# Kernel optimization log

Measured on AMD Instinct MI355X. Metric: run time of the kernel, lower is better.

The kernel has to match this reference:

```python
import jax, jax.numpy as jnp
import numpy as np
from jax import lax


def conv1x1(x, w, b):
    # x [B,Ci,H,W], w [Co,Ci], b [Co]
    return jnp.einsum('oi,bihw->bohw', w, x) + b[None, :, None, None]


def dil_conv_relu(x, w, b):
    # 3x3 conv, dilation 2, padding 2 (make_layers with dilation=True), then ReLU
    y = lax.conv_general_dilated(x, w, (1, 1), [(2, 2), (2, 2)], rhs_dilation=(2, 2),
                                 dimension_numbers=('NCHW', 'OIHW', 'NCHW'))
    return jax.nn.relu(y + b[None, :, None, None])


def conv1d_relu(x, w, b):
    # x [n,c,L], w [o,i,9], padding 4 -> same length; conv + ReLU (nn.Sequential(Conv2d, ReLU))
    y = lax.conv_general_dilated(x, w, (1,), [(4, 4)], dimension_numbers=('NCH', 'OIH', 'NCH'))
    return jax.nn.relu(y + b[None, :, None])


def dulr_pass(slices, w, b):
    # slices [L,n,c,m]; out[0]=slices[0]; out[i]=convrelu(out[i-1]) + slices[i]
    def step(carry, s):
        new = conv1d_relu(carry, w, b) + s
        return new, new
    _, rest = lax.scan(step, slices[0], slices[1:])
    return jnp.concatenate([slices[:1], rest], axis=0)


def conv_du(x, w, b):
    # down pass then up pass over rows (kernel (1,9) -> 1D conv along width)
    rows = jnp.moveaxis(x, 2, 0)            # [h,n,c,w]
    rows = dulr_pass(rows, w, b)
    rows = dulr_pass(rows[::-1], w, b)[::-1]
    return jnp.moveaxis(rows, 0, 2)


def conv_lr(x, w, b):
    # left-right then right-left over columns (kernel (9,1) -> 1D conv along height)
    cols = jnp.moveaxis(x, 3, 0)            # [w,n,c,h]
    cols = dulr_pass(cols, w, b)
    cols = dulr_pass(cols[::-1], w, b)[::-1]
    return jnp.moveaxis(cols, 0, 3)


def setup_inputs() -> dict:
    key = jax.random.key(0)
    ks = jax.random.split(key, 24)
    B, H, W = 4, 64, 64
    std = 0.01
    f32 = jnp.float32
    d = {}
    d['in_data'] = jax.random.normal(ks[0], (B, 1025, H, W), f32)
    d['wA'] = jax.random.normal(ks[1], (128, 1024), f32) * std
    d['bA'] = jax.random.normal(ks[2], (128,), f32) * std
    d['wB'] = jax.random.normal(ks[3], (128, 1024), f32) * std
    d['bB'] = jax.random.normal(ks[4], (128,), f32) * std
    d['wC'] = jax.random.normal(ks[5], (1024, 1024), f32) * std
    d['bC'] = jax.random.normal(ks[6], (1024,), f32) * std
    d['gamma'] = jnp.array(0.1, f32)
    chans = [(512, 1024), (512, 512), (512, 512), (256, 512), (128, 256), (64, 128)]
    for i, (co, ci) in enumerate(chans):
        d[f'bw{i+1}'] = jax.random.normal(ks[7 + 2 * i], (co, ci, 3, 3), f32) * std
        d[f'bb{i+1}'] = jax.random.normal(ks[8 + 2 * i], (co,), f32) * std
    d['du_w'] = jax.random.normal(ks[19], (64, 64, 9), f32) * std
    d['du_b'] = jax.random.normal(ks[20], (64,), f32) * std
    d['lr_w'] = jax.random.normal(ks[21], (64, 64, 9), f32) * std
    d['lr_b'] = jax.random.normal(ks[22], (64,), f32) * std
    d['ow'] = jax.random.normal(ks[23], (1, 64), f32) * std
    d['ob'] = jnp.zeros((1,), f32)
    return d


def reference(in_data, wA, bA, wB, bB, wC, bC, gamma,
              bw1, bb1, bw2, bb2, bw3, bb3, bw4, bb4, bw5, bb5, bw6, bb6,
              du_w, du_b, lr_w, lr_b, ow, ob):
    x = in_data[:, :1024]                   # [B,1024,H,W]
    f = in_data[:, 1024:1025]               # [B,1,H,W]
    B, C, H, W = x.shape
    N = H * W
    # appearance_A(x) -> query [B,128,N]
    q = conv1x1(x, wA, bA).reshape(B, 128, N)
    # f1024 = f broadcast to 1024 channels; flow_B(f1024) (1x1 conv) == f * sum_i wB[:,i] + bB
    k = (f * wB.sum(axis=1)[None, :, None, None] + bB[None, :, None, None]).reshape(B, 128, N)
    energy = jnp.einsum('bcn,bcm->bnm', q, k)           # [B,N,N] = q^T k
    att = jax.nn.softmax(energy, axis=-1)
    v = conv1x1(x, wC, bC).reshape(B, C, N)             # appearance_C
    out = jnp.einsum('bcj,bij->bci', v, att).reshape(B, C, H, W)  # bmm(v, att^T)
    x = gamma * out + x
    for w_, b_ in ((bw1, bb1), (bw2, bb2), (bw3, bb3), (bw4, bb4), (bw5, bb5), (bw6, bb6)):
        x = dil_conv_relu(x, w_, b_)
    x = conv_du(x, du_w, du_b)
    x = conv_lr(x, lr_w, lr_b)
    x = jax.nn.relu(conv1x1(x, ow, ob))                 # o_layer
    # F.upsample(scale_factor=8) default nearest
    x = jnp.repeat(jnp.repeat(x, 8, axis=2), 8, axis=3)
    return x
```

## Files before the change

### kernel.cpp

```cpp
#include <hip/hip_runtime.h>


#define NPIX 4096

typedef _Float16 f16;
typedef _Float16 f16x8 __attribute__((ext_vector_type(8)));
typedef _Float16 f16x4 __attribute__((ext_vector_type(4)));
typedef float f32x4 __attribute__((ext_vector_type(4)));

__device__ inline void async16(const void* g, void* l) {
  __builtin_amdgcn_global_load_lds(
      (const __attribute__((address_space(1))) unsigned int*)g,
      (__attribute__((address_space(3))) unsigned int*)l, 16, 0, 0);
}


__global__ void rf_zero(float* __restrict__ z) { z[threadIdx.x] = 0.f; }

__global__ void rf_s(const float* __restrict__ wB, const float* __restrict__ bA,
                     float* __restrict__ s_out, float* __restrict__ c0_out) {
  int c = threadIdx.x;
  const float* row = wB + (size_t)c * 1024;
  float acc = 0.f;
  for (int i = 0; i < 1024; ++i) acc += row[i];
  s_out[c] = acc;
  __shared__ float sh[128];
  sh[c] = acc * bA[c];
  __syncthreads();
  for (int off = 64; off > 0; off >>= 1) {
    if (c < off) sh[c] += sh[c + off];
    __syncthreads();
  }
  if (c == 0) c0_out[0] = sh[0];
}

__global__ void rf_u(const float* __restrict__ wA, const float* __restrict__ s,
                     float* __restrict__ u) {
  int i = blockIdx.x * 256 + threadIdx.x;
  float acc = 0.f;
  for (int c = 0; c < 128; ++c) acc += s[c] * wA[(size_t)c * 1024 + i];
  u[i] = acc;
}

__global__ void rf_fstat(const float* __restrict__ in, float* __restrict__ fstat) {
  int b = blockIdx.x;
  int t = threadIdx.x;
  const float* f = in + ((size_t)b * 1025 + 1024) * NPIX;
  float mx = -1e30f, mn = 1e30f;
  for (int j = t; j < NPIX; j += 256) {
    float v = f[j];
    mx = fmaxf(mx, v);
    mn = fminf(mn, v);
  }
  __shared__ float smx[256], smn[256];
  smx[t] = mx; smn[t] = mn;
  __syncthreads();
  for (int off = 128; off > 0; off >>= 1) {
    if (t < off) {
      smx[t] = fmaxf(smx[t], smx[t + off]);
      smn[t] = fminf(smn[t], smn[t + off]);
    }
    __syncthreads();
  }
  if (t == 0) { fstat[b] = smx[0]; fstat[4 + b] = smn[0]; }
}

__global__ __launch_bounds__(256) void rf_A(const float* __restrict__ in,
                                            const float* __restrict__ u,
                                            const float* __restrict__ c0p,
                                            const float* __restrict__ fst,
                                            float* __restrict__ A, float* __restrict__ M) {
  __shared__ float ul[1024];
  int b = blockIdx.y;
  int n = blockIdx.x * 256 + threadIdx.x;
  for (int s = threadIdx.x; s < 1024; s += 256) ul[s] = u[s];
  __syncthreads();
  const float* xp = in + (size_t)b * 1025 * NPIX + n;
  float acc = c0p[0];
#pragma unroll 8
  for (int i = 0; i < 1024; ++i) acc = fmaf(ul[i], xp[(size_t)i * NPIX], acc);
  A[b * NPIX + n] = acc;
  M[b * NPIX + n] = fmaxf(acc * fst[b], acc * fst[4 + b]);
}

__global__ void rf_Z(const float* __restrict__ in, const float* __restrict__ A,
                     const float* __restrict__ M, float* __restrict__ iZ) {
  int idx = blockIdx.x * 4 + (threadIdx.x >> 6);
  int lane = threadIdx.x & 63;
  int b = idx >> 12;
  const float* f = in + ((size_t)b * 1025 + 1024) * NPIX;
  float a = A[idx], m = M[idx];
  float acc = 0.f;
#pragma unroll 4
  for (int it = 0; it < 64; ++it) acc += __expf(a * f[lane + it * 64] - m);
  for (int off = 32; off > 0; off >>= 1) acc += __shfl_down(acc, off, 64);
  if (lane == 0) iZ[idx] = 1.0f / acc;
}


__global__ void rf_xsplit(const float* __restrict__ in, f16* __restrict__ xh) {
  __shared__ float tl[64][65];
  int nt = blockIdx.x, ct = blockIdx.y, b = blockIdx.z;
  int n0 = nt * 64, c0 = ct * 64;
  int tid = threadIdx.x;
  for (int s = tid; s < 4096; s += 256) {
    int r = s >> 6, c = s & 63;
    tl[r][c] = in[((size_t)b * 1025 + c0 + r) * NPIX + n0 + c];
  }
  __syncthreads();
  for (int s = tid; s < 512; s += 256) {
    int n = s >> 3, g = s & 7;
    f16x8 hb;
#pragma unroll
    for (int q = 0; q < 8; ++q) hb[q] = (f16)(16.f * tl[g * 8 + q][n]);
    size_t o = ((size_t)b * NPIX + n0 + n) * 1024 + c0 + g * 8;
    *(f16x8*)&xh[o] = hb;
  }
}


__global__ void rf_wC1(const float* __restrict__ wC, f16* __restrict__ wh) {
  int base = (blockIdx.x * 256 + threadIdx.x) * 8;
  f16x8 hb;
#pragma unroll
  for (int q = 0; q < 8; ++q) hb[q] = (f16)(256.f * wC[base + q]);
  *(f16x8*)&wh[base] = hb;
}


__global__ __launch_bounds__(256, 2) void rf_vgemmm(
    const f16* __restrict__ wh, const f16* __restrict__ xh,
    const float* __restrict__ bC, f16* __restrict__ vH) {
  __shared__ f16 sA[2][4096], sB[2][4096];
  const int tid = threadIdx.x;
  const int nb = blockIdx.x * 128, cb = blockIdx.y * 128, b = blockIdx.z;
  const int pA = tid & 127;
  const int wv = tid >> 6, lane = tid & 63;
  const int mrow = lane & 15, quad = lane >> 4;
  const int wm = (wv & 1) * 64, wn = (wv >> 1) * 64;
  const size_t abase = (size_t)(cb + pA) * 1024;
  const size_t bbase = ((size_t)b * NPIX + nb + pA) * 1024;
  f32x4 acc[4][4];
#pragma unroll
  for (int i = 0; i < 4; ++i)
#pragma unroll
    for (int j = 0; j < 4; ++j) acc[i][j] = (f32x4){0.f, 0.f, 0.f, 0.f};

  auto stage = [&](int k0, int pb) {
#pragma unroll
    for (int s = 0; s < 2; ++s) {
      const int cc = ((tid + 256 * s) >> 7) & 3;
      const int lb = ((tid & ~63) + 256 * s) * 8;
      async16(wh + abase + k0 + cc * 8, &sA[pb][lb]);
      async16(xh + bbase + k0 + cc * 8, &sB[pb][lb]);
    }
  };
  stage(0, 0);
  int p = 0;
  for (int k0 = 0; k0 < 1024; k0 += 32) {
    __syncthreads();
    if (k0 + 32 < 1024) stage(k0 + 32, p ^ 1);
    f16x8 fa[4], fb[4];
#pragma unroll
    for (int mi = 0; mi < 4; ++mi)
      fa[mi] = *(const f16x8*)&sA[p][(quad * 128 + wm + mi * 16 + mrow) * 8];
#pragma unroll
    for (int ni = 0; ni < 4; ++ni)
      fb[ni] = *(const f16x8*)&sB[p][(quad * 128 + wn + ni * 16 + mrow) * 8];
#pragma unroll
    for (int mi = 0; mi < 4; ++mi)
#pragma unroll
      for (int ni = 0; ni < 4; ++ni)
        acc[mi][ni] = __builtin_amdgcn_mfma_f32_16x16x32_f16(fa[mi], fb[ni], acc[mi][ni], 0, 0, 0);
    p ^= 1;
  }
  const float inv = 1.0f / 4096.0f;
#pragma unroll
  for (int mi = 0; mi < 4; ++mi) {
#pragma unroll
    for (int rg = 0; rg < 4; ++rg) {
      int c = cb + wm + mi * 16 + quad * 4 + rg;
      float bv = bC[c];
#pragma unroll
      for (int ni = 0; ni < 4; ++ni) {
        int j = nb + wn + ni * 16 + mrow;
        vH[((size_t)b * 1024 + c) * NPIX + j] =
            (f16)(16.f * (acc[mi][ni][rg] * inv + bv));
      }
    }
  }
}


__global__ __launch_bounds__(256, 2) void rf_attm(
    const f16* __restrict__ vH,
    const float* __restrict__ Aarr, const float* __restrict__ Marr,
    const float* __restrict__ iZ, const float* __restrict__ in,
    const float* __restrict__ gptr, f16* __restrict__ yH) {
  __shared__ f16 sAh[4096], sPh[4096];
  const int tid = threadIdx.x;
  const int ib = blockIdx.x * 128, cb = blockIdx.y * 128, b = blockIdx.z;
  const int pA = tid & 127;
  const int wv = tid >> 6, lane = tid & 63;
  const int mrow = lane & 15, quad = lane >> 4;
  const int wm = (wv & 1) * 64, wn = (wv >> 1) * 64;
  const size_t vbase = ((size_t)b * 1024 + cb + pA) * NPIX;
  const int ni_ = tid & 127;
  const int kc0 = tid >> 7;
  const float av = Aarr[b * NPIX + ib + ni_];
  const float mv = Marr[b * NPIX + ib + ni_];
  const float zv = iZ[b * NPIX + ib + ni_] * 16.f;
  const float* f = in + ((size_t)b * 1025 + 1024) * NPIX;
  f32x4 acc[4][4];
#pragma unroll
  for (int i = 0; i < 4; ++i)
#pragma unroll
    for (int j = 0; j < 4; ++j) acc[i][j] = (f32x4){0.f, 0.f, 0.f, 0.f};
  for (int j0 = 0; j0 < NPIX; j0 += 32) {
#pragma unroll
    for (int s = 0; s < 2; ++s) {
      const int cc = ((tid + 256 * s) >> 7) & 3;
      const int lb = ((tid & ~63) + 256 * s) * 8;
      async16(vH + vbase + j0 + cc * 8, &sAh[lb]);
    }
#pragma unroll
    for (int it = 0; it < 2; ++it) {
      const int kc = kc0 + 2 * it;
      const float4 fa = *(const float4*)&f[j0 + kc * 8];
      const float4 fb = *(const float4*)&f[j0 + kc * 8 + 4];
      const float fj[8] = {fa.x, fa.y, fa.z, fa.w, fb.x, fb.y, fb.z, fb.w};
      f16x8 ph;
#pragma unroll
      for (int q = 0; q < 8; ++q)
        ph[q] = (f16)(__expf(fmaf(av, fj[q], -mv)) * zv);
      *(f16x8*)&sPh[(kc * 128 + ni_) * 8] = ph;
    }
    __syncthreads();
    f16x8 fa[4], fb[4];
#pragma unroll
    for (int mi = 0; mi < 4; ++mi)
      fa[mi] = *(const f16x8*)&sAh[(quad * 128 + wm + mi * 16 + mrow) * 8];
#pragma unroll
    for (int ni = 0; ni < 4; ++ni)
      fb[ni] = *(const f16x8*)&sPh[(quad * 128 + wn + ni * 16 + mrow) * 8];
#pragma unroll
    for (int mi = 0; mi < 4; ++mi)
#pragma unroll
      for (int ni = 0; ni < 4; ++ni)
        acc[mi][ni] = __builtin_amdgcn_mfma_f32_16x16x32_f16(fa[mi], fb[ni], acc[mi][ni], 0, 0, 0);
    __syncthreads();
  }
  const float g = gptr[0];
  const float inv = 1.0f / 256.0f;
#pragma unroll
  for (int mi = 0; mi < 4; ++mi) {
    const int cbase = cb + wm + mi * 16 + quad * 4;
#pragma unroll
    for (int ni = 0; ni < 4; ++ni) {
      const int i = ib + wn + ni * 16 + mrow;
      f16x4 hv;
#pragma unroll
      for (int rg = 0; rg < 4; ++rg) {
        float xr = in[((size_t)b * 1025 + cbase + rg) * NPIX + i];
        hv[rg] = (f16)(16.f * (g * (acc[mi][ni][rg] * inv) + xr));
      }
      *(f16x4*)&yH[((size_t)b * NPIX + i) * 1024 + cbase] = hv;
    }
  }
}


__global__ void rf_wfragc(const float* __restrict__ w, f16* __restrict__ F,
                          int CI, int CO) {
  int gid = blockIdx.x * 256 + threadIdx.x;
  const int C16 = CO >> 4, KI = CI >> 5;
  const int total = 9 * KI * C16 * 64;
  if (gid >= total) return;
  int lane = gid & 63;
  int rest = gid >> 6;
  int c16 = rest % C16;
  int rest2 = rest / C16;
  int k = rest2 % KI;
  int t = rest2 / KI;
  int co = c16 * 16 + (lane & 15);
  int ci = k * 32 + (lane >> 4) * 8;
  f16x8 hb;
#pragma unroll
  for (int j = 0; j < 8; ++j)
    hb[j] = (f16)(256.0f * w[((size_t)co * CI + ci + j) * 9 + t]);
  *(f16x8*)&F[(size_t)gid * 8] = hb;
}


template <int BM, int BN, bool F32OUT>
__global__ __launch_bounds__(256, 2) void rf_mconv(
    const f16* __restrict__ xh, const f16* __restrict__ F,
    const float* __restrict__ bias, const float* __restrict__ zp,
    f16* __restrict__ oh, float* __restrict__ of, int CI, int CO) {
  constexpr int ROWS = BM / 64;
  constexpr int TPI = 4096 / BM;
  constexpr int HROWS = ROWS + 4;
  constexpr int COLP = 72;
  constexpr int CHUNKS = HROWS * 4 * COLP;
  constexpr int NSTG = (CHUNKS + 255) / 256;
  __shared__ f16 sA[2][NSTG * 2048];
  const int tid = threadIdx.x;
  const int blkpx = blockIdx.x;
  const int cob = blockIdx.y * BN;
  const int b = blkpx / TPI;
  const int h0 = (blkpx - b * TPI) * ROWS;

  const int wv = tid >> 6, lane = tid & 63;
  const int mrow = lane & 15, quad = lane >> 4;
  const int wm = (BN == 128) ? (wv & 1) * 64 : wv * 64;
  const int wn = (BN == 128) ? (wv >> 1) * 64 : 0;
  const int r_out = wm >> 6;
  const int KI = CI >> 5;
  const int C16 = CO >> 4;
  const int cb16 = (cob + wn) >> 4;

  f32x4 acc[4][4];
#pragma unroll
  for (int i = 0; i < 4; ++i)
#pragma unroll
    for (int j = 0; j < 4; ++j) acc[i][j] = (f32x4){0.f, 0.f, 0.f, 0.f};

  const f16* abase[NSTG];
  unsigned vmask = 0;
#pragma unroll
  for (int s = 0; s < NSTG; ++s) {
    int idx = tid + 256 * s;
    int rowks = idx / COLP;
    int col = idx - rowks * COLP;
    int r = rowks >> 2, ks = rowks & 3;
    int srow = h0 + r - 2, scol = col - 2;
    bool ok = (idx < CHUNKS) && ((unsigned)srow < 64u) && ((unsigned)scol < 64u);
    abase[s] = ok ? xh + (((size_t)b * 64 + srow) * 64 + scol) * CI + ks * 8
                  : (const f16*)zp;
    if (ok) vmask |= (1u << s);
  }
  auto stageA = [&](int k, int pb) {
#pragma unroll
    for (int s = 0; s < NSTG; ++s) {
      const f16* sp = abase[s] + (((vmask >> s) & 1u) ? k * 32 : 0);
      async16(sp, &sA[pb][((tid & ~63) + 256 * s) * 8]);
    }
  };

  const f16* Fb = F + ((size_t)cb16 * 64 + lane) * 8;

  stageA(0, 0);
  int p = 0;
  for (int k = 0; k < KI; ++k) {
    __syncthreads();
    if (k + 1 < KI) stageA(k + 1, p ^ 1);
#pragma unroll
    for (int t = 0; t < 9; ++t) {
      const int dh = (t / 3) * 2 - 2, dw = (t - (t / 3) * 3) * 2 - 2;
      f16x8 fb[4];
#pragma unroll
      for (int ni = 0; ni < 4; ++ni)
        fb[ni] = *(const f16x8*)(Fb + ((size_t)(t * KI + k) * C16 + ni) * 512);
      f16x8 fa[4];
#pragma unroll
      for (int mi = 0; mi < 4; ++mi)
        fa[mi] = *(const f16x8*)&sA[p][(((r_out + dh + 2) * 4 + quad) * COLP +
                                       mi * 16 + mrow + dw + 2) * 8];
#pragma unroll
      for (int mi = 0; mi < 4; ++mi)
#pragma unroll
        for (int ni = 0; ni < 4; ++ni)
          acc[mi][ni] = __builtin_amdgcn_mfma_f32_16x16x32_f16(fa[mi], fb[ni], acc[mi][ni], 0, 0, 0);
    }
    p ^= 1;
  }

  const float inv = 1.0f / 4096.0f;
  float bvs[4];
#pragma unroll
  for (int ni = 0; ni < 4; ++ni) bvs[ni] = bias[cob + wn + ni * 16 + mrow];
#pragma unroll
  for (int mi = 0; mi < 4; ++mi) {
#pragma unroll
    for (int rg = 0; rg < 4; ++rg) {
      int px = wm + mi * 16 + quad * 4 + rg;
      int hh = h0 + (px >> 6), wwp = px & 63;
#pragma unroll
      for (int ni = 0; ni < 4; ++ni) {
        int co = cob + wn + ni * 16 + mrow;
        float vv = fmaxf(acc[mi][ni][rg] * inv + bvs[ni], 0.f);
        if (F32OUT) {
          of[(((size_t)b * CO + co) * 64 + hh) * 64 + wwp] = vv;
        } else {
          oh[(((size_t)b * 64 + hh) * 64 + wwp) * CO + co] = (f16)(vv * 16.f);
        }
      }
    }
  }
}


__global__ void rf_wfrag(const float* __restrict__ w, f16* __restrict__ fh) {
  int gid = blockIdx.x * 256 + threadIdx.x;
  if (gid >= 4608) return;
  int lane = gid & 63;
  int rem = gid >> 6;
  int kc = rem & 1;
  int rem2 = rem >> 1;
  int t = rem2 % 9;
  int w4 = rem2 / 9;
  int co = w4 * 16 + (lane & 15);
  int cib = kc * 32 + (lane >> 4) * 8;
  f16x8 hb;
#pragma unroll
  for (int j = 0; j < 8; ++j)
    hb[j] = (f16)(256.f * w[((size_t)co * 64 + cib + j) * 9 + t]);
  *(f16x8*)&fh[(size_t)gid * 8] = hb;
}


__global__ __launch_bounds__(256, 1) void rf_mscan(
    const float* __restrict__ src, float* __restrict__ dst,
    const f16* __restrict__ fh, const float* __restrict__ bias, int dir) {
  __shared__ f16 ch[72 * 64];
  const int b = blockIdx.x;
  const int tid = threadIdx.x;
  const int wave = tid >> 6, lane = tid & 63;
  const int quad = lane >> 4, l15 = lane & 15;

  f16x8 Ah[9][2];
#pragma unroll
  for (int t = 0; t < 9; ++t)
#pragma unroll
    for (int kc = 0; kc < 2; ++kc)
      Ah[t][kc] = *(const f16x8*)&fh[(((wave * 9 + t) * 2 + kc) * 64 + lane) * 8];
  float bvs[4];
#pragma unroll
  for (int r = 0; r < 4; ++r) bvs[r] = bias[wave * 16 + quad * 4 + r];

  for (int s = tid; s < 2304; s += 256) ((unsigned*)ch)[s] = 0u;
  __syncthreads();

  const size_t sbase = (size_t)b * 64 * 4096;
  const int row0 = (dir > 0) ? 0 : 63;
  {
    int pos0 = tid & 63, cig = tid >> 6;
#pragma unroll
    for (int q = 0; q < 16; ++q) {
      int ci = cig * 16 + q;
      float v = src[sbase + (size_t)ci * 4096 + row0 * 64 + pos0];
      dst[sbase + (size_t)ci * 4096 + row0 * 64 + pos0] = v;
      int rowIdx = pos0 + 4;
      ch[rowIdx * 64 + (((ci >> 3) ^ (rowIdx & 7)) << 3) + (ci & 7)] = (f16)v;
    }
  }
  __syncthreads();

  const float inv = 1.0f / 256.0f;
  for (int s = 1; s < 64; ++s) {
    const int row = (dir > 0) ? s : 63 - s;
    float srow[4][4];
#pragma unroll
    for (int nt = 0; nt < 4; ++nt)
#pragma unroll
      for (int r = 0; r < 4; ++r)
        srow[nt][r] = src[sbase + (size_t)(wave * 16 + quad * 4 + r) * 4096 +
                          row * 64 + nt * 16 + l15];
    f32x4 acc[4];
#pragma unroll
    for (int nt = 0; nt < 4; ++nt) acc[nt] = (f32x4){0.f, 0.f, 0.f, 0.f};
#pragma unroll
    for (int t = 0; t < 9; ++t)
#pragma unroll
      for (int kc = 0; kc < 2; ++kc) {
#pragma unroll
        for (int nt = 0; nt < 4; ++nt) {
          int rowIdx = nt * 16 + l15 + t;
          int gr = kc * 4 + quad;
          f16x8 Bh = *(const f16x8*)&ch[rowIdx * 64 + ((gr ^ (rowIdx & 7)) << 3)];
          acc[nt] = __builtin_amdgcn_mfma_f32_16x16x32_f16(Ah[t][kc], Bh, acc[nt], 0, 0, 0);
        }
      }
    __syncthreads();
#pragma unroll
    for (int nt = 0; nt < 4; ++nt) {
      int pos = nt * 16 + l15;
      int rowIdx = pos + 4;
      f16x4 hv;
#pragma unroll
      for (int r = 0; r < 4; ++r) {
        float v = fmaxf(acc[nt][r] * inv + bvs[r], 0.f) + srow[nt][r];
        dst[sbase + (size_t)(wave * 16 + quad * 4 + r) * 4096 + row * 64 + pos] = v;
        hv[r] = (f16)v;
      }
      int ci0 = wave * 16 + quad * 4;
      *(f16x4*)&ch[rowIdx * 64 + (((ci0 >> 3) ^ (rowIdx & 7)) << 3) + (ci0 & 7)] = hv;
    }
    __syncthreads();
  }
}


__global__ void rf_transpose(const float* __restrict__ src, float* __restrict__ dst) {
  int bc = blockIdx.x;
  __shared__ float tl[64][65];
  int tid = threadIdx.x;
  const float* sp = src + (size_t)bc * 4096;
  float* dp = dst + (size_t)bc * 4096;
  for (int s = tid; s < 4096; s += 256) {
    int h = s >> 6, w = s & 63;
    tl[w][h] = sp[s];
  }
  __syncthreads();
  for (int s = tid; s < 4096; s += 256) dp[s] = tl[s >> 6][s & 63];
}


__global__ void rf_final(const float* __restrict__ t, const float* __restrict__ ow,
                         const float* __restrict__ ob, float* __restrict__ out) {
  int b = blockIdx.y;
  int s = blockIdx.x * 256 + threadIdx.x;
  int w = s >> 6, h = s & 63;
  float acc = ob[0];
  for (int c = 0; c < 64; ++c)
    acc += ow[c] * t[(((size_t)b * 64 + c) * 64 + w) * 64 + h];
  acc = fmaxf(acc, 0.f);
  float4 vv = make_float4(acc, acc, acc, acc);
  for (int dy = 0; dy < 8; ++dy) {
    float* dp = out + ((size_t)b * 512 + h * 8 + dy) * 512 + w * 8;
    *(float4*)dp = vv;
    *(float4*)(dp + 4) = vv;
  }
}


extern "C" void kernel_launch(void* const* d_in, const int* in_sizes, int n_in,
                              void* d_out, int out_size, void* d_ws, size_t ws_size,
                              hipStream_t stream) {
  const float* in    = (const float*)d_in[0];
  const float* wA    = (const float*)d_in[1];
  const float* bA    = (const float*)d_in[2];
  const float* wB    = (const float*)d_in[3];
  const float* wC    = (const float*)d_in[5];
  const float* bC    = (const float*)d_in[6];
  const float* gamma = (const float*)d_in[7];
  const float* bw1 = (const float*)d_in[8];  const float* bb1 = (const float*)d_in[9];
  const float* bw2 = (const float*)d_in[10]; const float* bb2 = (const float*)d_in[11];
  const float* bw3 = (const float*)d_in[12]; const float* bb3 = (const float*)d_in[13];
  const float* bw4 = (const float*)d_in[14]; const float* bb4 = (const float*)d_in[15];
  const float* bw5 = (const float*)d_in[16]; const float* bb5 = (const float*)d_in[17];
  const float* bw6 = (const float*)d_in[18]; const float* bb6 = (const float*)d_in[19];
  const float* du_w = (const float*)d_in[20]; const float* du_b = (const float*)d_in[21];
  const float* lr_w = (const float*)d_in[22]; const float* lr_b = (const float*)d_in[23];
  const float* ow   = (const float*)d_in[24]; const float* ob   = (const float*)d_in[25];
  float* out = (float*)d_out;
  float* ws = (float*)d_ws;

  f16* vH  = (f16*)(ws + 0);
  f16* xTh = (f16*)(ws + 4194304);
  f16* wCh = (f16*)(ws + 8388608);
  f16* yH  = (f16*)(ws + 16777216);
  f16* w1h = (f16*)(ws + 0);
  f16* c1H = (f16*)(ws + 2359296);
  f16* w3h = (f16*)(ws + 6553600);
  f16* w2h = (f16*)(ws + 16777216);
  f16* c2H = (f16*)(ws + 17956864);
  f16* w4h = (f16*)(ws + 22151168);
  f16* c4H = (f16*)(ws + 22740992);
  f16* c3H = c1H;
  f16* w5h = (f16*)(ws + 0);
  f16* c5H = (f16*)(ws + 147456);
  f16* w6h = (f16*)(ws + 1196032);
  float* tin = ws + 1232896;
  float* t0  = ws + 2281472;
  float* t1  = ws + 3330048;
  f16* duFh = (f16*)(ws + 4378624);
  f16* lrFh = (f16*)(ws + 4397056);
  float* sm = ws + 33554432;
  float* A_  = sm;
  float* M_  = sm + 16384;
  float* iZ  = sm + 32768;
  float* u_  = sm + 49152;
  float* s_  = sm + 50176;
  float* c0_ = sm + 50304;
  float* fst = sm + 50308;
  float* zp  = sm + 50432;

  rf_zero<<<1, 64, 0, stream>>>(zp);
  rf_s<<<1, 128, 0, stream>>>(wB, bA, s_, c0_);
  rf_u<<<4, 256, 0, stream>>>(wA, s_, u_);
  rf_fstat<<<4, 256, 0, stream>>>(in, fst);
  rf_A<<<dim3(16, 4), 256, 0, stream>>>(in, u_, c0_, fst, A_, M_);
  rf_Z<<<4096, 256, 0, stream>>>(in, A_, M_, iZ);
  rf_xsplit<<<dim3(64, 16, 4), 256, 0, stream>>>(in, xTh);
  rf_wC1<<<512, 256, 0, stream>>>(wC, wCh);
  rf_vgemmm<<<dim3(32, 8, 4), 256, 0, stream>>>(wCh, xTh, bC, vH);
  rf_attm<<<dim3(32, 8, 4), 256, 0, stream>>>(vH, A_, M_, iZ, in, gamma, yH);

  rf_wfragc<<<2304, 256, 0, stream>>>(bw1, w1h, 1024, 512);
  rf_wfragc<<<1152, 256, 0, stream>>>(bw3, w3h, 512, 512);
  rf_mconv<128, 128, false><<<dim3(128, 4), 256, 0, stream>>>(
      yH, w1h, bb1, zp, c1H, nullptr, 1024, 512);
  rf_wfragc<<<1152, 256, 0, stream>>>(bw2, w2h, 512, 512);
  rf_wfragc<<<576, 256, 0, stream>>>(bw4, w4h, 512, 256);
  rf_wfragc<<<144, 256, 0, stream>>>(bw5, w5h, 256, 128);
  rf_wfragc<<<36, 256, 0, stream>>>(bw6, w6h, 128, 64);
  rf_mconv<128, 128, false><<<dim3(128, 4), 256, 0, stream>>>(
      c1H, w2h, bb2, zp, c2H, nullptr, 512, 512);
  rf_mconv<128, 128, false><<<dim3(128, 4), 256, 0, stream>>>(
      c2H, w3h, bb3, zp, c3H, nullptr, 512, 512);
  rf_mconv<128, 128, false><<<dim3(128, 2), 256, 0, stream>>>(
      c3H, w4h, bb4, zp, c4H, nullptr, 512, 256);
  rf_wfrag<<<18, 256, 0, stream>>>(du_w, duFh);
  rf_wfrag<<<18, 256, 0, stream>>>(lr_w, lrFh);
  rf_mconv<128, 128, false><<<dim3(128, 1), 256, 0, stream>>>(
      c4H, w5h, bb5, zp, c5H, nullptr, 256, 128);
  rf_mconv<256, 64, true><<<dim3(64, 1), 256, 0, stream>>>(
      c5H, w6h, bb6, zp, nullptr, tin, 128, 64);

  rf_mscan<<<4, 256, 0, stream>>>(tin, t0, duFh, du_b, +1);
  rf_mscan<<<4, 256, 0, stream>>>(t0, t1, duFh, du_b, -1);
  rf_transpose<<<256, 256, 0, stream>>>(t1, t0);
  rf_mscan<<<4, 256, 0, stream>>>(t0, t1, lrFh, lr_b, +1);
  rf_mscan<<<4, 256, 0, stream>>>(t1, t0, lrFh, lr_b, -1);
  rf_final<<<dim3(16, 4), 256, 0, stream>>>(t0, ow, ob, out);
}
```

Before: 1.715 ms.

## Double-buffer attention GEMM, widen channel tile, move softmax normalization to epilogue

The attention-apply kernel now processes 256 channels per block instead of 128, with each wave owning 64 channels across all 128 pixels. This halves the redundant exp recomputation of the probability tile per channel block and halves the grid. LDS is double-buffered so the next V tile is loaded and P computed while MFMAs run on the current one, which removes one barrier per iteration. The exponent uses exp2 with prescaled constants, and the 1/Z normalization moves from each P element to the per-column epilogue. Unnormalized exp values stored in fp16 risk a narrower range, and the larger accumulator array raises register pressure.

```diff
diff --git a/kernel.cpp b/kernel.cpp
--- a/kernel.cpp
+++ b/kernel.cpp
@@ -197,72 +197,87 @@
     const float* __restrict__ Aarr, const float* __restrict__ Marr,
     const float* __restrict__ iZ, const float* __restrict__ in,
     const float* __restrict__ gptr, f16* __restrict__ yH) {
-  __shared__ f16 sAh[4096], sPh[4096];
+  __shared__ f16 sAh[2][8192];
+  __shared__ f16 sPh[2][4096];
   const int tid = threadIdx.x;
-  const int ib = blockIdx.x * 128, cb = blockIdx.y * 128, b = blockIdx.z;
-  const int pA = tid & 127;
+  const int ib = blockIdx.x * 128, cb = blockIdx.y * 256, b = blockIdx.z;
   const int wv = tid >> 6, lane = tid & 63;
   const int mrow = lane & 15, quad = lane >> 4;
-  const int wm = (wv & 1) * 64, wn = (wv >> 1) * 64;
-  const size_t vbase = ((size_t)b * 1024 + cb + pA) * NPIX;
+  const int wm = wv * 64;
   const int ni_ = tid & 127;
   const int kc0 = tid >> 7;
-  const float av = Aarr[b * NPIX + ib + ni_];
-  const float mv = Marr[b * NPIX + ib + ni_];
-  const float zv = iZ[b * NPIX + ib + ni_] * 16.f;
+  const float av2 = Aarr[b * NPIX + ib + ni_] * 1.44269504f;
+  const float mv2 = Marr[b * NPIX + ib + ni_] * 1.44269504f;
   const float* f = in + ((size_t)b * 1025 + 1024) * NPIX;
-  f32x4 acc[4][4];
+  const f16* vrow = vH + ((size_t)b * 1024 + cb + tid) * NPIX;
+
+  f32x4 acc[4][8];
 #pragma unroll
   for (int i = 0; i < 4; ++i)
 #pragma unroll
-    for (int j = 0; j < 4; ++j) acc[i][j] = (f32x4){0.f, 0.f, 0.f, 0.f};
-  for (int j0 = 0; j0 < NPIX; j0 += 32) {
-#pragma unroll
-    for (int s = 0; s < 2; ++s) {
-      const int cc = ((tid + 256 * s) >> 7) & 3;
-      const int lb = ((tid & ~63) + 256 * s) * 8;
-      async16(vH + vbase + j0 + cc * 8, &sAh[lb]);
-    }
+    for (int j = 0; j < 8; ++j) acc[i][j] = (f32x4){0.f, 0.f, 0.f, 0.f};
+
+  auto stage = [&](int j0, int pb) {
+#pragma unroll
+    for (int s = 0; s < 4; ++s)
+      async16(vrow + j0 + s * 8, &sAh[pb][(s * 256 + tid) * 8]);
+  };
+  auto doP = [&](int j0, int pb) {
 #pragma unroll
     for (int it = 0; it < 2; ++it) {
       const int kc = kc0 + 2 * it;
-      const float4 fa = *(const float4*)&f[j0 + kc * 8];
-      const float4 fb = *(const float4*)&f[j0 + kc * 8 + 4];
-      const float fj[8] = {fa.x, fa.y, fa.z, fa.w, fb.x, fb.y, fb.z, fb.w};
+      const float4 fa4 = *(const float4*)&f[j0 + kc * 8];
+      const float4 fb4 = *(const float4*)&f[j0 + kc * 8 + 4];
+      const float fj[8] = {fa4.x, fa4.y, fa4.z, fa4.w, fb4.x, fb4.y, fb4.z, fb4.w};
       f16x8 ph;
 #pragma unroll
       for (int q = 0; q < 8; ++q)
-        ph[q] = (f16)(__expf(fmaf(av, fj[q], -mv)) * zv);
-      *(f16x8*)&sPh[(kc * 128 + ni_) * 8] = ph;
-    }
+        ph[q] = (f16)exp2f(fmaf(av2, fj[q], -mv2));
+      *(f16x8*)&sPh[pb][(kc * 128 + ni_) * 8] = ph;
+    }
+  };
+
+  stage(0, 0);
+  doP(0, 0);
+  int p = 0;
+  for (int k = 0; k < 128; ++k) {
     __syncthreads();
-    f16x8 fa[4], fb[4];
+    f16x8 fa[4], fb[8];
 #pragma unroll
     for (int mi = 0; mi < 4; ++mi)
-      fa[mi] = *(const f16x8*)&sAh[(quad * 128 + wm + mi * 16 + mrow) * 8];
-#pragma unroll
-    for (int ni = 0; ni < 4; ++ni)
-      fb[ni] = *(const f16x8*)&sPh[(quad * 128 + wn + ni * 16 + mrow) * 8];
+      fa[mi] = *(const f16x8*)&sAh[p][(quad * 256 + wm + mi * 16 + mrow) * 8];
+#pragma unroll
+    for (int ni = 0; ni < 8; ++ni)
+      fb[ni] = *(const f16x8*)&sPh[p][(quad * 128 + ni * 16 + mrow) * 8];
+    if (k < 127) {
+      stage((k + 1) * 32, p ^ 1);
+      doP((k + 1) * 32, p ^ 1);
+    }
 #pragma unroll
     for (int mi = 0; mi < 4; ++mi)
 #pragma unroll
-      for (int ni = 0; ni < 4; ++ni)
+      for (int ni = 0; ni < 8; ++ni)
         acc[mi][ni] = __builtin_amdgcn_mfma_f32_16x16x32_f16(fa[mi], fb[ni], acc[mi][ni], 0, 0, 0);
-    __syncthreads();
-  }
+    p ^= 1;
+  }
+
   const float g = gptr[0];
-  const float inv = 1.0f / 256.0f;
+  const float inv16 = 1.0f / 16.0f;
+  float zvi[8];
+#pragma unroll
+  for (int ni = 0; ni < 8; ++ni)
+    zvi[ni] = iZ[b * NPIX + ib + ni * 16 + mrow] * inv16;
 #pragma unroll
   for (int mi = 0; mi < 4; ++mi) {
     const int cbase = cb + wm + mi * 16 + quad * 4;
 #pragma unroll
-    for (int ni = 0; ni < 4; ++ni) {
-      const int i = ib + wn + ni * 16 + mrow;
+    for (int ni = 0; ni < 8; ++ni) {
+      const int i = ib + ni * 16 + mrow;
       f16x4 hv;
 #pragma unroll
       for (int rg = 0; rg < 4; ++rg) {
         float xr = in[((size_t)b * 1025 + cbase + rg) * NPIX + i];
-        hv[rg] = (f16)(16.f * (g * (acc[mi][ni][rg] * inv) + xr));
+        hv[rg] = (f16)(16.f * (g * (acc[mi][ni][rg] * zvi[ni]) + xr));
       }
       *(f16x4*)&yH[((size_t)b * NPIX + i) * 1024 + cbase] = hv;
     }
@@ -595,7 +610,7 @@
   rf_xsplit<<<dim3(64, 16, 4), 256, 0, stream>>>(in, xTh);
   rf_wC1<<<512, 256, 0, stream>>>(wC, wCh);
   rf_vgemmm<<<dim3(32, 8, 4), 256, 0, stream>>>(wCh, xTh, bC, vH);
-  rf_attm<<<dim3(32, 8, 4), 256, 0, stream>>>(vH, A_, M_, iZ, in, gamma, yH);
+  rf_attm<<<dim3(32, 4, 4), 256, 0, stream>>>(vH, A_, M_, iZ, in, gamma, yH);
 
   rf_wfragc<<<2304, 256, 0, stream>>>(bw1, w1h, 1024, 512);
   rf_wfragc<<<1152, 256, 0, stream>>>(bw3, w3h, 512, 512);
```

Result: no change. 1.702 ms (-0.7%).
